# Performance work log

Hardware: AMD Instinct MI355X
Metric: run time of the kernel (lower is better)

Reference implementation:

```python
import jax, jax.numpy as jnp
import numpy as np

N, E, IN, H, G, OUT = 50000, 800000, 128, 128, 64, 10
HEADS, C = 4, 32  # per-head dim = H // HEADS so 4-head concat -> H (keeps chain dims consistent)


def setup_inputs() -> dict:
    key = jax.random.key(0)
    ks = jax.random.split(key, 16)
    p = lambda i, shape: jax.random.normal(ks[i], shape, jnp.float32) * 0.05
    return {
        "x": jax.random.normal(ks[0], (N, IN), jnp.float32),
        "edge_index": jax.random.randint(ks[1], (2, E), 0, N),
        "batch": jnp.sort(jax.random.randint(ks[2], (N,), 0, G)),
        "gcn_W": p(3, (IN, H)), "gcn_b": jnp.zeros((H,), jnp.float32),
        "gat_W": p(4, (H, HEADS * C)),
        "att_src": p(5, (HEADS, C)), "att_dst": p(6, (HEADS, C)),
        "gat_b": jnp.zeros((HEADS * C,), jnp.float32),
        "ec_W1": p(7, (2 * H, 128)), "ec_b1": jnp.zeros((128,), jnp.float32),
        "ec_W2": p(8, (128, H)), "ec_b2": jnp.zeros((H,), jnp.float32),
        "gin_W1": p(9, (H, 128)), "gin_b1": jnp.zeros((128,), jnp.float32),
        "gin_W2": p(10, (128, H)), "gin_b2": jnp.zeros((H,), jnp.float32),
        "gate_W1": p(11, (H, 128)), "gate_b1": jnp.zeros((128,), jnp.float32),
        "gate_W2": p(12, (128, 1)), "gate_b2": jnp.zeros((1,), jnp.float32),
        "fc_W": p(13, (H, OUT)), "fc_b": jnp.zeros((OUT,), jnp.float32),
    }


def reference(x, edge_index, batch, gcn_W, gcn_b, gat_W, att_src, att_dst, gat_b,
              ec_W1, ec_b1, ec_W2, ec_b2, gin_W1, gin_b1, gin_W2, gin_b2,
              gate_W1, gate_b1, gate_W2, gate_b2, fc_W, fc_b):
    src, dst = edge_index[0], edge_index[1]
    loop = jnp.arange(N)
    src_l = jnp.concatenate([src, loop])  # self loops for GCN / GAT
    dst_l = jnp.concatenate([dst, loop])

    deg = jax.ops.segment_sum(jnp.ones_like(dst_l, jnp.float32), dst_l, N)
    dinv = jnp.where(deg > 0, jax.lax.rsqrt(deg), 0.0)
    h = x @ gcn_W
    norm = dinv[src_l] * dinv[dst_l]  # [E+N]
    h = jax.ops.segment_sum(h[src_l] * norm[:, None], dst_l, N) + gcn_b
    h = jax.nn.relu(h)

    # ---- GATConv: 4 heads, per-target edge softmax, concat ----
    g = (h @ gat_W).reshape(N, HEADS, C)
    a_src = (g * att_src).sum(-1)  # [N, HEADS]
    a_dst = (g * att_dst).sum(-1)
    e = jax.nn.leaky_relu(a_src[src_l] + a_dst[dst_l], 0.2)  # [E+N, HEADS]
    e_max = jax.ops.segment_max(e, dst_l, N)
    e = jnp.exp(e - e_max[dst_l])
    e_sum = jax.ops.segment_sum(e, dst_l, N)
    alpha = e / (e_sum[dst_l] + 1e-16)
    h = jax.ops.segment_sum(g[src_l] * alpha[..., None], dst_l, N).reshape(N, HEADS * C) + gat_b
    h = jax.nn.elu(h)

    # ---- EdgeConv: nn([x_i, x_j - x_i]) with max aggregation ----
    msg = jnp.concatenate([h[dst], h[src] - h[dst]], axis=-1)  # [E, 2H]
    msg = jax.nn.relu(msg @ ec_W1 + ec_b1) @ ec_W2 + ec_b2
    agg = jax.ops.segment_max(msg, dst, N)
    h = jax.nn.relu(jnp.where(jnp.isfinite(agg), agg, 0.0))  # isolated nodes -> 0 (PyG scatter-max fill)

    # ---- GINConv (eps=0): nn(x + sum_j x_j) ----
    s = h + jax.ops.segment_sum(h[src], dst, N)
    h = jax.nn.relu(jax.nn.relu(s @ gin_W1 + gin_b1) @ gin_W2 + gin_b2)

    # ---- GlobalAttention pooling: per-graph softmax gating ----
    gate = jax.nn.relu(h @ gate_W1 + gate_b1) @ gate_W2 + gate_b2  # [N, 1]
    gmax = jax.ops.segment_max(gate, batch, G)
    ge = jnp.exp(gate - gmax[batch])
    gsum = jax.ops.segment_sum(ge, batch, G)
    w = ge / (gsum[batch] + 1e-16)
    pooled = jax.ops.segment_sum(w * h, batch, G)  # [G, H]

    out = pooled @ fc_W + fc_b
    return jax.nn.log_softmax(out, axis=1)
```

## Files before the change

### kernel.cpp

```cpp
#include <hip/hip_runtime.h>

#define H 128
#define OUTD 10

typedef short bf16x8 __attribute__((ext_vector_type(8)));
typedef float f32x4 __attribute__((ext_vector_type(4)));

__device__ __forceinline__ unsigned short f2bf(float x) {
  unsigned u = __float_as_uint(x);
  u += 0x7fffu + ((u >> 16) & 1u);
  return (unsigned short)(u >> 16);
}
__device__ __forceinline__ unsigned pack2bf(float a, float b) {
  return (unsigned)f2bf(a) | ((unsigned)f2bf(b) << 16);
}
__device__ __forceinline__ float bf2f(unsigned short u) {
  return __uint_as_float(((unsigned)u) << 16);
}
__device__ __forceinline__ float bflo(unsigned u) { return __uint_as_float(u << 16); }
__device__ __forceinline__ float bfhi(unsigned u) { return __uint_as_float(u & 0xffff0000u); }

__device__ __forceinline__ unsigned fenc(float x) {
  unsigned u = __float_as_uint(x);
  return (u & 0x80000000u) ? ~u : (u | 0x80000000u);
}
__device__ __forceinline__ float fdec(unsigned u) {
  u = (u & 0x80000000u) ? (u & 0x7fffffffu) : ~u;
  return __uint_as_float(u);
}

__global__ void prep_w(const float* __restrict__ gcnW, const float* __restrict__ gatW,
                       const float* __restrict__ ecW1, const float* __restrict__ ecW2,
                       const float* __restrict__ ginW1, const float* __restrict__ ginW2,
                       const float* __restrict__ gtW1, unsigned short* __restrict__ WT) {
  int f = blockIdx.x * 256 + threadIdx.x;
  if (f >= 8 * 16384) return;
  int m = f >> 14, idx = f & 16383;
  int j = idx >> 7, k = idx & 127;
  int src = k * 128 + j;
  float v;
  switch (m) {
    case 0: v = gcnW[src]; break;
    case 1: v = gatW[src]; break;
    case 2: v = ecW1[src] - ecW1[16384 + src]; break;
    case 3: v = ecW1[16384 + src]; break;
    case 4: v = ecW2[src]; break;
    case 5: v = ginW1[src]; break;
    case 6: v = ginW2[src]; break;
    default: v = gtW1[src]; break;
  }
  WT[f] = f2bf(v);
}

template <int IN_BF, int RELU, int BIAS>
__global__ __launch_bounds__(256) void dense_mfma(const void* __restrict__ Xv,
                                                  const unsigned short* __restrict__ WT,
                                                  const float* __restrict__ bias,
                                                  unsigned short* __restrict__ Y, int n) {
  __shared__ unsigned short tile[64][136];
  const int tid = threadIdx.x, lane = tid & 63, wave = tid >> 6;
  const int jl = lane & 15, kg = lane >> 4;
  const int base = blockIdx.x * 64;
  if (base >= n) return;
  const int nr = min(64, n - base);
  if (IN_BF) {
    const uint4* X4 = (const uint4*)Xv;
#pragma unroll
    for (int it = 0; it < 4; ++it) {
      int f = it * 256 + tid, r = f >> 4, q = f & 15;
      if (r < nr) *(uint4*)&tile[r][q * 8] = X4[(size_t)(base + r) * 16 + q];
    }
  } else {
    const float* X = (const float*)Xv;
#pragma unroll
    for (int it = 0; it < 16; ++it) {
      int f = it * 256 + tid, r = f >> 6, kp = f & 63;
      if (r < nr) {
        float2 v = *(const float2*)&X[(size_t)(base + r) * H + 2 * kp];
        *(unsigned*)&tile[r][2 * kp] = pack2bf(v.x, v.y);
      }
    }
  }
  __syncthreads();
  bf16x8 afrag[4];
#pragma unroll
  for (int kk = 0; kk < 4; ++kk)
    afrag[kk] = *(const bf16x8*)&tile[wave * 16 + jl][kk * 32 + kg * 8];
  f32x4 acc[8];
#pragma unroll
  for (int jt = 0; jt < 8; ++jt) {
    f32x4 c = {0.f, 0.f, 0.f, 0.f};
#pragma unroll
    for (int kk = 0; kk < 4; ++kk) {
      bf16x8 bf = *(const bf16x8*)&WT[(size_t)(jt * 16 + jl) * H + kk * 32 + kg * 8];
      c = __builtin_amdgcn_mfma_f32_16x16x32_bf16(afrag[kk], bf, c, 0, 0, 0);
    }
    if (BIAS) {
      float bb = bias[jt * 16 + jl];
#pragma unroll
      for (int r = 0; r < 4; ++r) c[r] += bb;
    }
    if (RELU) {
#pragma unroll
      for (int r = 0; r < 4; ++r) c[r] = fmaxf(c[r], 0.f);
    }
    acc[jt] = c;
  }
  __syncthreads();
#pragma unroll
  for (int jt = 0; jt < 8; ++jt)
#pragma unroll
    for (int r = 0; r < 4; ++r) tile[wave * 16 + kg * 4 + r][jt * 16 + jl] = f2bf(acc[jt][r]);
  __syncthreads();
#pragma unroll
  for (int it = 0; it < 4; ++it) {
    int f = it * 256 + tid, r = f >> 4, q = f & 15;
    if (r < nr) *(uint4*)&Y[(size_t)(base + r) * H + q * 8] = *(const uint4*)&tile[r][q * 8];
  }
}

__global__ __launch_bounds__(256) void dense_dual(const unsigned short* __restrict__ X,
                                                  const unsigned short* __restrict__ WT1,
                                                  const unsigned short* __restrict__ WT2,
                                                  const float* __restrict__ bias2,
                                                  unsigned short* __restrict__ Y1,
                                                  unsigned short* __restrict__ Y2, int n) {
  __shared__ unsigned short tile[64][136];
  const int tid = threadIdx.x, lane = tid & 63, wave = tid >> 6;
  const int jl = lane & 15, kg = lane >> 4;
  const int base = blockIdx.x * 64;
  if (base >= n) return;
  const int nr = min(64, n - base);
  const uint4* X4 = (const uint4*)X;
#pragma unroll
  for (int it = 0; it < 4; ++it) {
    int f = it * 256 + tid, r = f >> 4, q = f & 15;
    if (r < nr) *(uint4*)&tile[r][q * 8] = X4[(size_t)(base + r) * 16 + q];
  }
  __syncthreads();
  bf16x8 afrag[4];
#pragma unroll
  for (int kk = 0; kk < 4; ++kk)
    afrag[kk] = *(const bf16x8*)&tile[wave * 16 + jl][kk * 32 + kg * 8];
  f32x4 acc[8];
#pragma unroll
  for (int jt = 0; jt < 8; ++jt) {
    f32x4 c = {0.f, 0.f, 0.f, 0.f};
#pragma unroll
    for (int kk = 0; kk < 4; ++kk) {
      bf16x8 bf = *(const bf16x8*)&WT1[(size_t)(jt * 16 + jl) * H + kk * 32 + kg * 8];
      c = __builtin_amdgcn_mfma_f32_16x16x32_bf16(afrag[kk], bf, c, 0, 0, 0);
    }
    acc[jt] = c;
  }
  __syncthreads();
#pragma unroll
  for (int jt = 0; jt < 8; ++jt)
#pragma unroll
    for (int r = 0; r < 4; ++r) tile[wave * 16 + kg * 4 + r][jt * 16 + jl] = f2bf(acc[jt][r]);
  __syncthreads();
#pragma unroll
  for (int it = 0; it < 4; ++it) {
    int f = it * 256 + tid, r = f >> 4, q = f & 15;
    if (r < nr) *(uint4*)&Y1[(size_t)(base + r) * H + q * 8] = *(const uint4*)&tile[r][q * 8];
  }
  __syncthreads();
#pragma unroll
  for (int jt = 0; jt < 8; ++jt) {
    f32x4 c = {0.f, 0.f, 0.f, 0.f};
#pragma unroll
    for (int kk = 0; kk < 4; ++kk) {
      bf16x8 bf = *(const bf16x8*)&WT2[(size_t)(jt * 16 + jl) * H + kk * 32 + kg * 8];
      c = __builtin_amdgcn_mfma_f32_16x16x32_bf16(afrag[kk], bf, c, 0, 0, 0);
// ... 165 lines not shown
  for (int off = 1; off < 1024; off <<= 1) {
    int v = (t >= off) ? ls[t - off] : 0;
    __syncthreads();
    ls[t] += v;
    __syncthreads();
  }
  int run = (t > 0) ? ls[t - 1] : 0;
  for (int i = a; i < b; ++i) {
    row_ptr[i] = run;
    run += cnt[i];
  }
  if (t == 1023) row_ptr[n] = ls[1023];
}
__global__ void copy_int(const int* __restrict__ a, int* __restrict__ b, int n) {
  int i = blockIdx.x * 256 + threadIdx.x;
  if (i < n) b[i] = a[i];
}
__global__ void csr_fill(const int* __restrict__ ei, int* __restrict__ cursor,
                         int* __restrict__ csr_src, int* __restrict__ csr_dst, int E) {
  int e = blockIdx.x * 256 + threadIdx.x;
  if (e >= E) return;
  int s = ei[e], d = ei[(size_t)E + e];
  int p = atomicAdd(&cursor[d], 1);
  csr_src[p] = s;
  csr_dst[p] = d;
}
__global__ void dinv_kernel(const int* __restrict__ row_ptr, float* __restrict__ dinv, int n) {
  int i = blockIdx.x * 256 + threadIdx.x;
  if (i < n) dinv[i] = rsqrtf((float)(1 + row_ptr[i + 1] - row_ptr[i]));
}
__global__ void fill_u32(unsigned* p, unsigned v, size_t n) {
  size_t i = (size_t)blockIdx.x * 256 + threadIdx.x;
  if (i < n) p[i] = v;
}

__global__ __launch_bounds__(256) void gcn_gather(const unsigned short* __restrict__ h,
                                                  const float* __restrict__ dinv,
                                                  const int* __restrict__ row_ptr,
                                                  const int* __restrict__ csr_src,
                                                  const float* __restrict__ bias,
                                                  unsigned short* __restrict__ out, int n) {
  int node = blockIdx.x * 4 + (threadIdx.x >> 6);
  int lane = threadIdx.x & 63;
  if (node >= n) return;
  const unsigned* hu = (const unsigned*)h;
  float di = dinv[node];
  unsigned v = hu[(size_t)node * 64 + lane];
  float t0 = bflo(v) * di, t1 = bfhi(v) * di;
  int a = row_ptr[node], b = row_ptr[node + 1];
  int e = a;
  for (; e + 8 <= b; e += 8) {
    int sx[8];
#pragma unroll
    for (int i = 0; i < 8; ++i) sx[i] = csr_src[e + i];
    unsigned w[8];
    float dd[8];
#pragma unroll
    for (int i = 0; i < 8; ++i) w[i] = hu[(size_t)sx[i] * 64 + lane];
#pragma unroll
    for (int i = 0; i < 8; ++i) dd[i] = dinv[sx[i]];
#pragma unroll
    for (int i = 0; i < 8; ++i) {
      t0 = fmaf(bflo(w[i]), dd[i], t0);
      t1 = fmaf(bfhi(w[i]), dd[i], t1);
    }
  }
  for (; e < b; ++e) {
    int s = csr_src[e];
    float ds = dinv[s];
    unsigned w = hu[(size_t)s * 64 + lane];
    t0 = fmaf(bflo(w), ds, t0);
    t1 = fmaf(bfhi(w), ds, t1);
  }
  float y0 = fmaxf(fmaf(t0, di, bias[lane * 2]), 0.f);
  float y1 = fmaxf(fmaf(t1, di, bias[lane * 2 + 1]), 0.f);
  ((unsigned*)out)[(size_t)node * 64 + lane] = pack2bf(y0, y1);
}

__global__ void att_pre(const unsigned short* __restrict__ g, const float* __restrict__ attS,
                        const float* __restrict__ attD, float* __restrict__ asrc,
                        float* __restrict__ adst, int n) {
  int t = blockIdx.x * 256 + threadIdx.x;
  if (t >= n * 4) return;
  int i = t >> 2, hd = t & 3;
  const unsigned* gr = (const unsigned*)(g + (size_t)i * H + hd * 32);
  float s1 = 0.f, s2 = 0.f;
#pragma unroll
  for (int p = 0; p < 16; ++p) {
    unsigned u = gr[p];
    float a = bflo(u), b = bfhi(u);
    s1 = fmaf(a, attS[hd * 32 + 2 * p], fmaf(b, attS[hd * 32 + 2 * p + 1], s1));
    s2 = fmaf(a, attD[hd * 32 + 2 * p], fmaf(b, attD[hd * 32 + 2 * p + 1], s2));
  }
  asrc[t] = s1;
  adst[t] = s2;
}

__device__ __forceinline__ float lrelu_exp(float v) {
  v = v > 0.f ? v : 0.2f * v;
  return __expf(v);
}

__global__ __launch_bounds__(256) void gat_gather(const unsigned short* __restrict__ g,
                                                  const float* __restrict__ asrc,
                                                  const float* __restrict__ adst,
                                                  const int* __restrict__ row_ptr,
                                                  const int* __restrict__ csr_src,
                                                  const float* __restrict__ bias,
                                                  unsigned short* __restrict__ out, int n) {
  int node = blockIdx.x * 4 + (threadIdx.x >> 6);
  int lane = threadIdx.x & 63;
  if (node >= n) return;
  const int hd = lane >> 4;
  const unsigned* gu = (const unsigned*)g;
  float adc = adst[node * 4 + hd];
  float w = lrelu_exp(asrc[node * 4 + hd] + adc);
  unsigned u = gu[(size_t)node * 64 + lane];
  float acc0 = w * bflo(u), acc1 = w * bfhi(u), wsum = w;
  int a = row_ptr[node], b = row_ptr[node + 1];
  int e = a;
  for (; e + 8 <= b; e += 8) {
    int sx[8];
#pragma unroll
    for (int i = 0; i < 8; ++i) sx[i] = csr_src[e + i];
    unsigned uu[8];
#pragma unroll
    for (int i = 0; i < 8; ++i) uu[i] = gu[(size_t)sx[i] * 64 + lane];
    float ww[8];
#pragma unroll
    for (int i = 0; i < 8; ++i) ww[i] = lrelu_exp(asrc[sx[i] * 4 + hd] + adc);
#pragma unroll
    for (int i = 0; i < 8; ++i) {
      acc0 = fmaf(ww[i], bflo(uu[i]), acc0);
      acc1 = fmaf(ww[i], bfhi(uu[i]), acc1);
      wsum += ww[i];
    }
  }
  for (; e < b; ++e) {
    int s = csr_src[e];
    unsigned us = gu[(size_t)s * 64 + lane];
    float we = lrelu_exp(asrc[s * 4 + hd] + adc);
    acc0 = fmaf(we, bflo(us), acc0);
    acc1 = fmaf(we, bfhi(us), acc1);
    wsum += we;
  }
  float inv = 1.f / (wsum + 1e-16f);
  float r0 = acc0 * inv + bias[2 * lane];
  float r1 = acc1 * inv + bias[2 * lane + 1];
  r0 = r0 > 0.f ? r0 : expm1f(r0);
  r1 = r1 > 0.f ? r1 : expm1f(r1);
  ((unsigned*)out)[(size_t)node * 64 + lane] = pack2bf(r0, r1);
}

__global__ __launch_bounds__(256) void edgeconv_tile(const unsigned short* __restrict__ A,
                                                     const unsigned short* __restrict__ Bm,
                                                     const int* __restrict__ csr_src,
                                                     const int* __restrict__ csr_dst,
                                                     const unsigned short* __restrict__ W2T,
                                                     const float* __restrict__ b2,
                                                     unsigned* __restrict__ hec, int E) {
  __shared__ unsigned short buf[2][64][140];
  __shared__ int dbuf[2][64];
  const int tid = threadIdx.x, lane = tid & 63, wave = tid >> 6;
  const int jl = lane & 15, kg = lane >> 4;
  const int srow = tid >> 2, sq = tid & 3;
  float b2v[8];
#pragma unroll
  for (int jt = 0; jt < 8; ++jt) b2v[jt] = b2[jt * 16 + jl];

  const int tiles = (E + 63) >> 6;
  int t = blockIdx.x;
  if (t >= tiles) return;
  int cur = 0;
  {
    int base = t << 6;
    int ne = min(64, E - base);
    uint2 pk[8];
    if (srow < ne) {
      int d = csr_dst[base + srow], s = csr_src[base + srow];
      const uint2* Ar = (const uint2*)(A + (size_t)d * H + sq * 32);
      const uint2* Br = (const uint2*)(Bm + (size_t)s * H + sq * 32);
#pragma unroll
      for (int i = 0; i < 8; ++i) {
        uint2 va = Ar[i], vb = Br[i];
        pk[i].x = pack2bf(fmaxf(bflo(va.x) + bflo(vb.x), 0.f), fmaxf(bfhi(va.x) + bfhi(vb.x), 0.f));
        pk[i].y = pack2bf(fmaxf(bflo(va.y) + bflo(vb.y), 0.f), fmaxf(bfhi(va.y) + bfhi(vb.y), 0.f));
      }
    } else {
#pragma unroll
      for (int i = 0; i < 8; ++i) pk[i] = {0u, 0u};
    }
#pragma unroll
    for (int i = 0; i < 8; ++i) *(uint2*)&buf[0][srow][sq * 32 + i * 4] = pk[i];
    if (sq == 0) dbuf[0][srow] = (srow < ne) ? csr_dst[base + srow] : -1;
  }
  __syncthreads();

  for (; t < tiles; t += gridDim.x) {
    const int nt = t + gridDim.x;
    const bool havenext = nt < tiles;
    uint2 pk[8];
    if (havenext) {
      int base = nt << 6;
      int ne = min(64, E - base);
      if (srow < ne) {
        int d = csr_dst[base + srow], s = csr_src[base + srow];
        const uint2* Ar = (const uint2*)(A + (size_t)d * H + sq * 32);
        const uint2* Br = (const uint2*)(Bm + (size_t)s * H + sq * 32);
#pragma unroll
        for (int i = 0; i < 8; ++i) {
          uint2 va = Ar[i], vb = Br[i];
          pk[i].x =
              pack2bf(fmaxf(bflo(va.x) + bflo(vb.x), 0.f), fmaxf(bfhi(va.x) + bfhi(vb.x), 0.f));
          pk[i].y =
              pack2bf(fmaxf(bflo(va.y) + bflo(vb.y), 0.f), fmaxf(bfhi(va.y) + bfhi(vb.y), 0.f));
        }
      } else {
#pragma unroll
        for (int i = 0; i < 8; ++i) pk[i] = {0u, 0u};
      }
    }
    bf16x8 af[4];
#pragma unroll
    for (int kk = 0; kk < 4; ++kk)
      af[kk] = *(const bf16x8*)&buf[cur][wave * 16 + jl][kk * 32 + kg * 8];
    const int r0 = wave * 16 + kg * 4;
    const int d0 = dbuf[cur][r0 + 0], d1 = dbuf[cur][r0 + 1];
    const int d2 = dbuf[cur][r0 + 2], d3 = dbuf[cur][r0 + 3];
    f32x4 acc[8];
#pragma unroll
    for (int jt = 0; jt < 8; ++jt) {
      f32x4 c = {0.f, 0.f, 0.f, 0.f};
#pragma unroll
      for (int kk = 0; kk < 4; ++kk) {
        bf16x8 wf = *(const bf16x8*)&W2T[(size_t)(jt * 16 + jl) * H + kk * 32 + kg * 8];
        c = __builtin_amdgcn_mfma_f32_16x16x32_bf16(af[kk], wf, c, 0, 0, 0);
      }
      acc[jt] = c;
    }
    if (havenext) {
      int base = nt << 6;
      int ne = min(64, E - base);
#pragma unroll
      for (int i = 0; i < 8; ++i) *(uint2*)&buf[cur ^ 1][srow][sq * 32 + i * 4] = pk[i];
      if (sq == 0) dbuf[cur ^ 1][srow] = (srow < ne) ? csr_dst[base + srow] : -1;
    }
    __syncthreads();
#pragma unroll
    for (int jt = 0; jt < 8; ++jt) {
      const int col = jt * 16 + jl;
      f32x4 c = acc[jt];
      int cd = d0;
      float m = c[0];
      if (d1 != cd) {
        if (cd >= 0) atomicMax(&hec[(size_t)cd * H + col], fenc(m + b2v[jt]));
        cd = d1;
        m = c[1];
      } else
        m = fmaxf(m, c[1]);
      if (d2 != cd) {
        if (cd >= 0) atomicMax(&hec[(size_t)cd * H + col], fenc(m + b2v[jt]));
        cd = d2;
        m = c[2];
      } else
        m = fmaxf(m, c[2]);
      if (d3 != cd) {
        if (cd >= 0) atomicMax(&hec[(size_t)cd * H + col], fenc(m + b2v[jt]));
        cd = d3;
        m = c[3];
      } else
        m = fmaxf(m, c[3]);
      if (cd >= 0) atomicMax(&hec[(size_t)cd * H + col], fenc(m + b2v[jt]));
    }
    cur ^= 1;
  }
}

__global__ void ec_decode(const unsigned* __restrict__ hec, unsigned short* __restrict__ out,
                          size_t half) {
  size_t i = (size_t)blockIdx.x * 256 + threadIdx.x;
  if (i < half) {
    uint2 v = *(const uint2*)&hec[i * 2];
    ((unsigned*)out)[i] = pack2bf(fdec(v.x), fdec(v.y));
  }
}

__global__ __launch_bounds__(256) void gin_gather(const unsigned short* __restrict__ h,
                                                  const int* __restrict__ row_ptr,
                                                  const int* __restrict__ csr_src,
                                                  unsigned short* __restrict__ out, int n) {
  int node = blockIdx.x * 4 + (threadIdx.x >> 6);
  int lane = threadIdx.x & 63;
  if (node >= n) return;
  const unsigned* hu = (const unsigned*)h;
  unsigned v = hu[(size_t)node * 64 + lane];
  float t0 = bflo(v), t1 = bfhi(v);
  int a = row_ptr[node], b = row_ptr[node + 1];
  int e = a;
  for (; e + 8 <= b; e += 8) {
    int sx[8];
#pragma unroll
    for (int i = 0; i < 8; ++i) sx[i] = csr_src[e + i];
    unsigned w[8];
#pragma unroll
    for (int i = 0; i < 8; ++i) w[i] = hu[(size_t)sx[i] * 64 + lane];
#pragma unroll
    for (int i = 0; i < 8; ++i) {
      t0 += bflo(w[i]);
      t1 += bfhi(w[i]);
    }
  }
  for (; e < b; ++e) {
    int s = csr_src[e];
    unsigned w = hu[(size_t)s * 64 + lane];
    t0 += bflo(w);
    t1 += bfhi(w);
  }
  ((unsigned*)out)[(size_t)node * 64 + lane] = pack2bf(t0, t1);
}

__global__ void starts_kernel(const int* __restrict__ batch, int* __restrict__ starts, int n,
                              int G) {
  int i = blockIdx.x * 256 + threadIdx.x;
  if (i >= n) return;
  int b = batch[i];
  int bp = (i == 0) ? -1 : batch[i - 1];
  for (int g = bp + 1; g <= b; ++g) starts[g] = i;
  if (i == n - 1)
    for (int g = b + 1; g <= G; ++g) starts[g] = n;
}
__global__ __launch_bounds__(256) void pool_fused(float* __restrict__ gate,
                                                  const unsigned short* __restrict__ h4,
                                                  const int* __restrict__ starts,
                                                  const float* __restrict__ fcW,
                                                  const float* __restrict__ fcB,
                                                  float* __restrict__ out) {
  __shared__ float red[256];
  __shared__ float pl[128];
  int g = blockIdx.x, t = threadIdx.x;
  int s0 = starts[g], s1 = starts[g + 1];
  float m = -1e30f;
  for (int i = s0 + t; i < s1; i += 256) m = fmaxf(m, gate[i]);
  red[t] = m;
  __syncthreads();
  for (int off = 128; off; off >>= 1) {
    if (t < off) red[t] = fmaxf(red[t], red[t + off]);
    __syncthreads();
  }
  m = red[0];
  __syncthreads();
  float sm = 0.f;
  for (int i = s0 + t; i < s1; i += 256) {
    float ge = __expf(gate[i] - m);
    gate[i] = ge;
    sm += ge;
  }
  red[t] = sm;
  __syncthreads();
  for (int off = 128; off; off >>= 1) {
    if (t < off) red[t] += red[t + off];
    __syncthreads();
  }
  float inv = 1.f / (red[0] + 1e-16f);
  __syncthreads();
  int c = t & 127, half = t >> 7;
  float acc = 0.f;
  for (int i = s0 + half; i < s1; i += 2) acc = fmaf(gate[i], bf2f(h4[(size_t)i * H + c]), acc);
  red[t] = acc;
  __syncthreads();
  if (t < 128) pl[t] = (red[t] + red[t + 128]) * inv;
  __syncthreads();
  if (t < OUTD) {
    float o = fcB[t];
    for (int k = 0; k < 128; ++k) o = fmaf(pl[k], fcW[k * OUTD + t], o);
    red[t] = o;
  }
  __syncthreads();
  if (t == 0) {
    float mm = -1e30f;
    for (int j = 0; j < OUTD; ++j) mm = fmaxf(mm, red[j]);
    float s = 0.f;
    for (int j = 0; j < OUTD; ++j) s += __expf(red[j] - mm);
    float l = logf(s);
    for (int j = 0; j < OUTD; ++j) out[g * OUTD + j] = red[j] - mm - l;
  }
}

extern "C" void kernel_launch(void* const* d_in, const int* in_sizes, int n_in, void* d_out,
                              int out_size, void* d_ws, size_t ws_size, hipStream_t stream) {
  const float* x = (const float*)d_in[0];
  const int* ei = (const int*)d_in[1];
  const int* batch = (const int*)d_in[2];
  const float* gcnW = (const float*)d_in[3];
  const float* gcnB = (const float*)d_in[4];
  const float* gatW = (const float*)d_in[5];
  const float* attS = (const float*)d_in[6];
  const float* attD = (const float*)d_in[7];
  const float* gatB = (const float*)d_in[8];
  const float* ecW1 = (const float*)d_in[9];
  const float* ecB1 = (const float*)d_in[10];
  const float* ecW2 = (const float*)d_in[11];
  const float* ecB2 = (const float*)d_in[12];
  const float* ginW1 = (const float*)d_in[13];
  const float* ginB1 = (const float*)d_in[14];
  const float* ginW2 = (const float*)d_in[15];
  const float* ginB2 = (const float*)d_in[16];
  const float* gtW1 = (const float*)d_in[17];
  const float* gtB1 = (const float*)d_in[18];
  const float* gtW2 = (const float*)d_in[19];
  const float* gtB2 = (const float*)d_in[20];
  const float* fcW = (const float*)d_in[21];
  const float* fcB = (const float*)d_in[22];

  const int N = in_sizes[0] / H;
  const int E = in_sizes[1] / 2;
  const int G = out_size / OUTD;
  const size_t NH = (size_t)N * H;

  auto align16 = [](char* p) { return (char*)(((uintptr_t)p + 15) & ~(uintptr_t)15); };
  char* p = (char*)d_ws;
  unsigned* hec = (unsigned*)p;      p += NH * 4;
  float* dinv = (float*)p;           p += (size_t)N * 4;
  float* asrc = (float*)p;           p += (size_t)4 * N * 4;
  float* adst = (float*)p;           p += (size_t)4 * N * 4;
  float* gate = (float*)p;           p += (size_t)N * 4;
  int* starts = (int*)p;             p += (size_t)(G + 1) * 4;
  int* cnt = (int*)p;                p += (size_t)N * 4;
  int* row_ptr = (int*)p;            p += (size_t)(N + 1) * 4;
  int* cursor = (int*)p;             p += (size_t)N * 4;
  int* csr_src = (int*)p;            p += (size_t)E * 4;
  int* csr_dst = (int*)p;            p += (size_t)E * 4;
  p = align16(p);
  unsigned short* WT = (unsigned short*)p;  p += (size_t)8 * 16384 * 2;
  p = align16(p);
  unsigned short* T0 = (unsigned short*)p;  p += NH * 2;
  p = align16(p);
  unsigned short* T1 = (unsigned short*)p;  p += NH * 2;
  p = align16(p);
  unsigned short* T2 = (unsigned short*)p;  p += NH * 2;

  const unsigned short* gcnT = WT;
  const unsigned short* gatT = WT + 16384;
  const unsigned short* WaT = WT + 2 * 16384;
  const unsigned short* WbT = WT + 3 * 16384;
  const unsigned short* W2T = WT + 4 * 16384;
  const unsigned short* gin1T = WT + 5 * 16384;
  const unsigned short* gin2T = WT + 6 * 16384;
  const unsigned short* gt1T = WT + 7 * 16384;

  const int gN = (N + 255) / 256;
  const int gNH = (int)((NH + 255) / 256);
  const int gE = (E + 255) / 256;
  const int gDense = (N + 63) / 64;
  const int gW4 = (N + 3) / 4;

  prep_w<<<(8 * 16384 + 255) / 256, 256, 0, stream>>>(gcnW, gatW, ecW1, ecW2, ginW1, ginW2,
                                                      gtW1, WT);
  zero_int<<<gN, 256, 0, stream>>>(cnt, N);
  csr_count<<<gE, 256, 0, stream>>>(ei, cnt, E);
  scan50k<<<1, 1024, 0, stream>>>(cnt, row_ptr, N);
  copy_int<<<gN, 256, 0, stream>>>(row_ptr, cursor, N);
  csr_fill<<<gE, 256, 0, stream>>>(ei, cursor, csr_src, csr_dst, E);
  dinv_kernel<<<gN, 256, 0, stream>>>(row_ptr, dinv, N);

  dense_mfma<0, 0, 0><<<gDense, 256, 0, stream>>>(x, gcnT, nullptr, T0, N);
  gcn_gather<<<gW4, 256, 0, stream>>>(T0, dinv, row_ptr, csr_src, gcnB, T1, N);

  dense_mfma<1, 0, 0><<<gDense, 256, 0, stream>>>(T1, gatT, nullptr, T2, N);
  att_pre<<<(N * 4 + 255) / 256, 256, 0, stream>>>(T2, attS, attD, asrc, adst, N);
  gat_gather<<<gW4, 256, 0, stream>>>(T2, asrc, adst, row_ptr, csr_src, gatB, T0, N);

  dense_dual<<<gDense, 256, 0, stream>>>(T0, WaT, WbT, ecB1, T1, T2, N);
  fill_u32<<<gNH, 256, 0, stream>>>(hec, 0x80000000u, NH);
  edgeconv_tile<<<2048, 256, 0, stream>>>(T1, T2, csr_src, csr_dst, W2T, ecB2, hec, E);
  ec_decode<<<(int)((NH / 2 + 255) / 256), 256, 0, stream>>>(hec, T0, NH / 2);

  gin_gather<<<gW4, 256, 0, stream>>>(T0, row_ptr, csr_src, T1, N);
  dense_chain<<<gDense, 256, 0, stream>>>(T1, gin1T, ginB1, gin2T, ginB2, T2, N);

  dense_gate<<<gDense, 256, 0, stream>>>(T2, gt1T, gtB1, gtW2, gtB2, gate, N);
  starts_kernel<<<gN, 256, 0, stream>>>(batch, starts, N, G);
  pool_fused<<<G, 256, 0, stream>>>(gate, T2, starts, fcW, fcB, (float*)d_out);
}
```

Before: 813.6 us.

## Aggregate EdgeConv max per destination in LDS slots before global atomics

Edges in each 64-edge tile are sorted by destination, so the kernel now runs a wave-level scan that assigns each distinct destination in the tile to one of up to 16 shared-memory slots. Partial maxima go through LDS atomicMax, and a single pass then flushes each slot to global memory. Destinations whose whole CSR range lies inside the tile get a plain store; the others still use a global atomicMax. This cuts global atomic traffic, at the cost of an extra barrier, the scan, and LDS atomics in every tile.

```diff
diff --git a/kernel.cpp b/kernel.cpp
--- a/kernel.cpp
+++ b/kernel.cpp
@@ -494,17 +494,26 @@
                                                      const unsigned short* __restrict__ Bm,
                                                      const int* __restrict__ csr_src,
                                                      const int* __restrict__ csr_dst,
+                                                     const int* __restrict__ row_ptr,
                                                      const unsigned short* __restrict__ W2T,
                                                      const float* __restrict__ b2,
                                                      unsigned* __restrict__ hec, int E) {
   __shared__ unsigned short buf[2][64][140];
   __shared__ int dbuf[2][64];
+  __shared__ unsigned slots[16][128];
+  __shared__ int slotmap[2][64];
+  __shared__ int slot_dst2[2][16];
+  __shared__ int slot_comp2[2][16];
+  __shared__ int nslots2[2];
   const int tid = threadIdx.x, lane = tid & 63, wave = tid >> 6;
   const int jl = lane & 15, kg = lane >> 4;
   const int srow = tid >> 2, sq = tid & 3;
   float b2v[8];
 #pragma unroll
   for (int jt = 0; jt < 8; ++jt) b2v[jt] = b2[jt * 16 + jl];
+  const float b2c = b2[tid & 127];
+
+  for (int i = tid; i < 16 * 128; i += 256) ((unsigned*)slots)[i] = 0;
 
   const int tiles = (E + 63) >> 6;
   int t = blockIdx.x;
@@ -535,14 +544,16 @@
   __syncthreads();
 
   for (; t < tiles; t += gridDim.x) {
+    const int base = t << 6;
+    const int ne = min(64, E - base);
     const int nt = t + gridDim.x;
     const bool havenext = nt < tiles;
     uint2 pk[8];
     if (havenext) {
-      int base = nt << 6;
-      int ne = min(64, E - base);
-      if (srow < ne) {
-        int d = csr_dst[base + srow], s = csr_src[base + srow];
+      int nbase = nt << 6;
+      int nne = min(64, E - nbase);
+      if (srow < nne) {
+        int d = csr_dst[nbase + srow], s = csr_src[nbase + srow];
         const uint2* Ar = (const uint2*)(A + (size_t)d * H + sq * 32);
         const uint2* Br = (const uint2*)(Bm + (size_t)s * H + sq * 32);
 #pragma unroll
@@ -562,9 +573,6 @@
 #pragma unroll
     for (int kk = 0; kk < 4; ++kk)
       af[kk] = *(const bf16x8*)&buf[cur][wave * 16 + jl][kk * 32 + kg * 8];
-    const int r0 = wave * 16 + kg * 4;
-    const int d0 = dbuf[cur][r0 + 0], d1 = dbuf[cur][r0 + 1];
-    const int d2 = dbuf[cur][r0 + 2], d3 = dbuf[cur][r0 + 3];
     f32x4 acc[8];
 #pragma unroll
     for (int jt = 0; jt < 8; ++jt) {
@@ -577,38 +585,89 @@
       acc[jt] = c;
     }
     if (havenext) {
-      int base = nt << 6;
-      int ne = min(64, E - base);
+      int nbase = nt << 6;
+      int nne = min(64, E - nbase);
 #pragma unroll
       for (int i = 0; i < 8; ++i) *(uint2*)&buf[cur ^ 1][srow][sq * 32 + i * 4] = pk[i];
-      if (sq == 0) dbuf[cur ^ 1][srow] = (srow < ne) ? csr_dst[base + srow] : -1;
+      if (sq == 0) dbuf[cur ^ 1][srow] = (srow < nne) ? csr_dst[nbase + srow] : -1;
+    }
+    if (wave == 0) {
+      int r = lane;
+      int d = dbuf[cur][r];
+      int dp = (r == 0) ? -1234567 : dbuf[cur][r - 1];
+      int start = (r < ne && d != dp) ? 1 : 0;
+      int ps = start;
+#pragma unroll
+      for (int off = 1; off < 64; off <<= 1) {
+        int v = __shfl_up(ps, off);
+        if (lane >= off) ps += v;
+      }
+      int slot = ps - 1;
+      slotmap[cur][r] = (r < ne) ? slot : 255;
+      if (start && slot < 16) {
+        slot_dst2[cur][slot] = d;
+        int e0 = row_ptr[d], e1 = row_ptr[d + 1];
+        slot_comp2[cur][slot] = (e0 >= base && e1 <= base + ne) ? 1 : 0;
+      }
+      if (r == 63) nslots2[cur] = ps;
     }
     __syncthreads();
-#pragma unroll
-    for (int jt = 0; jt < 8; ++jt) {
-      const int col = jt * 16 + jl;
-      f32x4 c = acc[jt];
-      int cd = d0;
-      float m = c[0];
-      if (d1 != cd) {
-        if (cd >= 0) atomicMax(&hec[(size_t)cd * H + col], fenc(m + b2v[jt]));
-        cd = d1;
-        m = c[1];
-      } else
-        m = fmaxf(m, c[1]);
-      if (d2 != cd) {
-        if (cd >= 0) atomicMax(&hec[(size_t)cd * H + col], fenc(m + b2v[jt]));
-        cd = d2;
-        m = c[2];
-      } else
-        m = fmaxf(m, c[2]);
-      if (d3 != cd) {
-        if (cd >= 0) atomicMax(&hec[(size_t)cd * H + col], fenc(m + b2v[jt]));
-        cd = d3;
-        m = c[3];
-      } else
-        m = fmaxf(m, c[3]);
-      if (cd >= 0) atomicMax(&hec[(size_t)cd * H + col], fenc(m + b2v[jt]));
+    {
+      const int r0 = wave * 16 + kg * 4;
+      int dd[4], ss[4];
+#pragma unroll
+      for (int r = 0; r < 4; ++r) {
+        dd[r] = dbuf[cur][r0 + r];
+        ss[r] = slotmap[cur][r0 + r];
+      }
+#pragma unroll
+      for (int jt = 0; jt < 8; ++jt) {
+        const int col = jt * 16 + jl;
+        f32x4 c = acc[jt];
+        int cd = dd[0], cs = ss[0];
+        float cm = c[0];
+#pragma unroll
+        for (int r = 1; r < 4; ++r) {
+          if (dd[r] == cd) {
+            cm = fmaxf(cm, c[r]);
+          } else {
+            if (cd >= 0) {
+              if (cs < 16)
+                atomicMax(&slots[cs][col], fenc(cm));
+              else
+                atomicMax(&hec[(size_t)cd * H + col], fenc(cm + b2v[jt]));
+            }
+            cd = dd[r];
+            cs = ss[r];
+            cm = c[r];
+          }
+        }
+        if (cd >= 0) {
+          if (cs < 16)
+            atomicMax(&slots[cs][col], fenc(cm));
+          else
+            atomicMax(&hec[(size_t)cd * H + col], fenc(cm + b2v[jt]));
+        }
+      }
+    }
+    __syncthreads();
+    {
+      int ns = min(nslots2[cur], 16);
+      int col = tid & 127, sb = tid >> 7;
+#pragma unroll
+      for (int k = 0; k < 8; ++k) {
+        int s = sb + k * 2;
+        if (s < ns) {
+          unsigned v = slots[s][col];
+          slots[s][col] = 0;
+          float f = fdec(v) + b2c;
+          size_t off = (size_t)slot_dst2[cur][s] * H + col;
+          if (slot_comp2[cur][s])
+            hec[off] = fenc(fmaxf(f, 0.f));
+          else
+            atomicMax(&hec[off], fenc(f));
+        }
+      }
     }
     cur ^= 1;
   }
@@ -810,7 +869,7 @@
 
   dense_dual<<<gDense, 256, 0, stream>>>(T0, WaT, WbT, ecB1, T1, T2, N);
   fill_u32<<<gNH, 256, 0, stream>>>(hec, 0x80000000u, NH);
-  edgeconv_tile<<<2048, 256, 0, stream>>>(T1, T2, csr_src, csr_dst, W2T, ecB2, hec, E);
+  edgeconv_tile<<<2048, 256, 0, stream>>>(T1, T2, csr_src, csr_dst, row_ptr, W2T, ecB2, hec, E);
   ec_decode<<<(int)((NH / 2 + 255) / 256), 256, 0, stream>>>(hec, T0, NH / 2);
 
   gin_gather<<<gW4, 256, 0, stream>>>(T0, row_ptr, csr_src, T1, N);
```

After: 844.3 us. 1.04x slower.

## Split EdgeConv into gather/add-relu message kernel and streaming MFMA max kernel

Applied to the files above, without the earlier changes.

When workspace allows, EdgeConv is split into two kernels. The first gathers the two per-node projections, adds them, applies relu and writes an E×128 bf16 message buffer. The second streams that buffer contiguously through the MFMA and atomic-max stage. The aim is to take the irregular random gathers out of the MFMA loop. The price is writing and re-reading about 200MB of intermediate data plus an extra launch. The fused kernel also now interleaves the atomics with the MFMAs instead of holding all accumulators first, and uses a smaller LDS pad.

```diff
diff --git a/kernel.cpp b/kernel.cpp
--- a/kernel.cpp
+++ b/kernel.cpp
@@ -19,6 +19,9 @@
 }
 __device__ __forceinline__ float bflo(unsigned u) { return __uint_as_float(u << 16); }
 __device__ __forceinline__ float bfhi(unsigned u) { return __uint_as_float(u & 0xffff0000u); }
+__device__ __forceinline__ unsigned addrelu2(unsigned a, unsigned b) {
+  return pack2bf(fmaxf(bflo(a) + bflo(b), 0.f), fmaxf(bfhi(a) + bfhi(b), 0.f));
+}
 
 __device__ __forceinline__ unsigned fenc(float x) {
   unsigned u = __float_as_uint(x);
@@ -490,14 +493,36 @@
   ((unsigned*)out)[(size_t)node * 64 + lane] = pack2bf(r0, r1);
 }
 
-__global__ __launch_bounds__(256) void edgeconv_tile(const unsigned short* __restrict__ A,
-                                                     const unsigned short* __restrict__ Bm,
-                                                     const int* __restrict__ csr_src,
-                                                     const int* __restrict__ csr_dst,
-                                                     const unsigned short* __restrict__ W2T,
-                                                     const float* __restrict__ b2,
-                                                     unsigned* __restrict__ hec, int E) {
-  __shared__ unsigned short buf[2][64][140];
+__global__ __launch_bounds__(256) void ec_msg(const unsigned short* __restrict__ A,
+                                              const unsigned short* __restrict__ Bm,
+                                              const int* __restrict__ csr_src,
+                                              const int* __restrict__ csr_dst,
+                                              unsigned short* __restrict__ msg, int E) {
+  const int tid = threadIdx.x;
+  const int qid = tid >> 4;
+  const int ql = tid & 15;
+  for (int e0 = blockIdx.x * 16; e0 < E; e0 += gridDim.x * 16) {
+    int e = e0 + qid;
+    if (e < E) {
+      int d = csr_dst[e], s = csr_src[e];
+      uint4 va = *(const uint4*)(A + (size_t)d * H + ql * 8);
+      uint4 vb = *(const uint4*)(Bm + (size_t)s * H + ql * 8);
+      uint4 o;
+      o.x = addrelu2(va.x, vb.x);
+      o.y = addrelu2(va.y, vb.y);
+      o.z = addrelu2(va.z, vb.z);
+      o.w = addrelu2(va.w, vb.w);
+      *(uint4*)(msg + (size_t)e * H + ql * 8) = o;
+    }
+  }
+}
+
+__global__ __launch_bounds__(256) void edgeconv_stream(const unsigned short* __restrict__ msg,
+                                                       const int* __restrict__ csr_dst,
+                                                       const unsigned short* __restrict__ W2T,
+                                                       const float* __restrict__ b2,
+                                                       unsigned* __restrict__ hec, int E) {
+  __shared__ unsigned short buf[2][64][136];
   __shared__ int dbuf[2][64];
   const int tid = threadIdx.x, lane = tid & 63, wave = tid >> 6;
   const int jl = lane & 15, kg = lane >> 4;
@@ -513,23 +538,17 @@
   {
     int base = t << 6;
     int ne = min(64, E - base);
-    uint2 pk[8];
+    uint4 pk[4];
     if (srow < ne) {
-      int d = csr_dst[base + srow], s = csr_src[base + srow];
-      const uint2* Ar = (const uint2*)(A + (size_t)d * H + sq * 32);
-      const uint2* Br = (const uint2*)(Bm + (size_t)s * H + sq * 32);
-#pragma unroll
-      for (int i = 0; i < 8; ++i) {
-        uint2 va = Ar[i], vb = Br[i];
-        pk[i].x = pack2bf(fmaxf(bflo(va.x) + bflo(vb.x), 0.f), fmaxf(bfhi(va.x) + bfhi(vb.x), 0.f));
-        pk[i].y = pack2bf(fmaxf(bflo(va.y) + bflo(vb.y), 0.f), fmaxf(bfhi(va.y) + bfhi(vb.y), 0.f));
-      }
+#pragma unroll
+      for (int i = 0; i < 4; ++i)
+        pk[i] = *(const uint4*)&msg[(size_t)(base + srow) * H + sq * 32 + i * 8];
     } else {
 #pragma unroll
-      for (int i = 0; i < 8; ++i) pk[i] = {0u, 0u};
-    }
-#pragma unroll
-    for (int i = 0; i < 8; ++i) *(uint2*)&buf[0][srow][sq * 32 + i * 4] = pk[i];
+      for (int i = 0; i < 4; ++i) pk[i] = {0u, 0u, 0u, 0u};
+    }
+#pragma unroll
+    for (int i = 0; i < 4; ++i) *(uint4*)&buf[0][srow][sq * 32 + i * 8] = pk[i];
     if (sq == 0) dbuf[0][srow] = (srow < ne) ? csr_dst[base + srow] : -1;
   }
   __syncthreads();
@@ -537,25 +556,18 @@
   for (; t < tiles; t += gridDim.x) {
     const int nt = t + gridDim.x;
     const bool havenext = nt < tiles;
-    uint2 pk[8];
+    uint4 pk[4];
+    int nne = 0;
     if (havenext) {
-      int base = nt << 6;
-      int ne = min(64, E - base);
-      if (srow < ne) {
-        int d = csr_dst[base + srow], s = csr_src[base + srow];
-        const uint2* Ar = (const uint2*)(A + (size_t)d * H + sq * 32);
-        const uint2* Br = (const uint2*)(Bm + (size_t)s * H + sq * 32);
-#pragma unroll
-        for (int i = 0; i < 8; ++i) {
-          uint2 va = Ar[i], vb = Br[i];
-          pk[i].x =
-              pack2bf(fmaxf(bflo(va.x) + bflo(vb.x), 0.f), fmaxf(bfhi(va.x) + bfhi(vb.x), 0.f));
-          pk[i].y =
-              pack2bf(fmaxf(bflo(va.y) + bflo(vb.y), 0.f), fmaxf(bfhi(va.y) + bfhi(vb.y), 0.f));
-        }
+      int nbase = nt << 6;
+      nne = min(64, E - nbase);
+      if (srow < nne) {
+#pragma unroll
+        for (int i = 0; i < 4; ++i)
+          pk[i] = *(const uint4*)&msg[(size_t)(nbase + srow) * H + sq * 32 + i * 8];
       } else {
 #pragma unroll
-        for (int i = 0; i < 8; ++i) pk[i] = {0u, 0u};
+        for (int i = 0; i < 4; ++i) pk[i] = {0u, 0u, 0u, 0u};
       }
     }
     bf16x8 af[4];
@@ -565,7 +577,6 @@
     const int r0 = wave * 16 + kg * 4;
     const int d0 = dbuf[cur][r0 + 0], d1 = dbuf[cur][r0 + 1];
     const int d2 = dbuf[cur][r0 + 2], d3 = dbuf[cur][r0 + 3];
-    f32x4 acc[8];
 #pragma unroll
     for (int jt = 0; jt < 8; ++jt) {
       f32x4 c = {0.f, 0.f, 0.f, 0.f};
@@ -574,20 +585,7 @@
         bf16x8 wf = *(const bf16x8*)&W2T[(size_t)(jt * 16 + jl) * H + kk * 32 + kg * 8];
         c = __builtin_amdgcn_mfma_f32_16x16x32_bf16(af[kk], wf, c, 0, 0, 0);
       }
-      acc[jt] = c;
-    }
-    if (havenext) {
-      int base = nt << 6;
-      int ne = min(64, E - base);
-#pragma unroll
-      for (int i = 0; i < 8; ++i) *(uint2*)&buf[cur ^ 1][srow][sq * 32 + i * 4] = pk[i];
-      if (sq == 0) dbuf[cur ^ 1][srow] = (srow < ne) ? csr_dst[base + srow] : -1;
-    }
-    __syncthreads();
-#pragma unroll
-    for (int jt = 0; jt < 8; ++jt) {
       const int col = jt * 16 + jl;
-      f32x4 c = acc[jt];
       int cd = d0;
       float m = c[0];
       if (d1 != cd) {
@@ -610,6 +608,129 @@
         m = fmaxf(m, c[3]);
       if (cd >= 0) atomicMax(&hec[(size_t)cd * H + col], fenc(m + b2v[jt]));
     }
+    if (havenext) {
+      int nbase = nt << 6;
+#pragma unroll
+      for (int i = 0; i < 4; ++i) *(uint4*)&buf[cur ^ 1][srow][sq * 32 + i * 8] = pk[i];
+      if (sq == 0) dbuf[cur ^ 1][srow] = (srow < nne) ? csr_dst[nbase + srow] : -1;
+    }
+    __syncthreads();
+    cur ^= 1;
+  }
+}
+
+__global__ __launch_bounds__(256) void edgeconv_tile(const unsigned short* __restrict__ A,
+                                                     const unsigned short* __restrict__ Bm,
+                                                     const int* __restrict__ csr_src,
+                                                     const int* __restrict__ csr_dst,
+                                                     const unsigned short* __restrict__ W2T,
+                                                     const float* __restrict__ b2,
+                                                     unsigned* __restrict__ hec, int E) {
+  __shared__ unsigned short buf[2][64][136];
+  __shared__ int dbuf[2][64];
+  const int tid = threadIdx.x, lane = tid & 63, wave = tid >> 6;
+  const int jl = lane & 15, kg = lane >> 4;
+  const int srow = tid >> 2, sq = tid & 3;
+  float b2v[8];
+#pragma unroll
+  for (int jt = 0; jt < 8; ++jt) b2v[jt] = b2[jt * 16 + jl];
+
+  const int tiles = (E + 63) >> 6;
+  int t = blockIdx.x;
+  if (t >= tiles) return;
+  int cur = 0;
+  {
+    int base = t << 6;
+    int ne = min(64, E - base);
+    uint2 pk[8];
+    if (srow < ne) {
+      int d = csr_dst[base + srow], s = csr_src[base + srow];
+      const uint2* Ar = (const uint2*)(A + (size_t)d * H + sq * 32);
+      const uint2* Br = (const uint2*)(Bm + (size_t)s * H + sq * 32);
+#pragma unroll
+      for (int i = 0; i < 8; ++i) {
+        uint2 va = Ar[i], vb = Br[i];
+        pk[i].x = addrelu2(va.x, vb.x);
+        pk[i].y = addrelu2(va.y, vb.y);
+      }
+    } else {
+#pragma unroll
+      for (int i = 0; i < 8; ++i) pk[i] = {0u, 0u};
+    }
+#pragma unroll
+    for (int i = 0; i < 8; ++i) *(uint2*)&buf[0][srow][sq * 32 + i * 4] = pk[i];
+    if (sq == 0) dbuf[0][srow] = (srow < ne) ? csr_dst[base + srow] : -1;
+  }
+  __syncthreads();
+
+  for (; t < tiles; t += gridDim.x) {
+    const int nt = t + gridDim.x;
+    const bool havenext = nt < tiles;
+    uint2 pk[8];
+    if (havenext) {
+      int base = nt << 6;
+      int ne = min(64, E - base);
+      if (srow < ne) {
+        int d = csr_dst[base + srow], s = csr_src[base + srow];
+        const uint2* Ar = (const uint2*)(A + (size_t)d * H + sq * 32);
+        const uint2* Br = (const uint2*)(Bm + (size_t)s * H + sq * 32);
+#pragma unroll
+        for (int i = 0; i < 8; ++i) {
+          uint2 va = Ar[i], vb = Br[i];
+          pk[i].x = addrelu2(va.x, vb.x);
+          pk[i].y = addrelu2(va.y, vb.y);
+        }
+      } else {
+#pragma unroll
+        for (int i = 0; i < 8; ++i) pk[i] = {0u, 0u};
+      }
+    }
+    bf16x8 af[4];
+#pragma unroll
+    for (int kk = 0; kk < 4; ++kk)
+      af[kk] = *(const bf16x8*)&buf[cur][wave * 16 + jl][kk * 32 + kg * 8];
+    const int r0 = wave * 16 + kg * 4;
+    const int d0 = dbuf[cur][r0 + 0], d1 = dbuf[cur][r0 + 1];
+    const int d2 = dbuf[cur][r0 + 2], d3 = dbuf[cur][r0 + 3];
+#pragma unroll
+    for (int jt = 0; jt < 8; ++jt) {
+      f32x4 c = {0.f, 0.f, 0.f, 0.f};
+#pragma unroll
+      for (int kk = 0; kk < 4; ++kk) {
+        bf16x8 wf = *(const bf16x8*)&W2T[(size_t)(jt * 16 + jl) * H + kk * 32 + kg * 8];
+        c = __builtin_amdgcn_mfma_f32_16x16x32_bf16(af[kk], wf, c, 0, 0, 0);
+      }
+      const int col = jt * 16 + jl;
+      int cd = d0;
+      float m = c[0];
+      if (d1 != cd) {
+        if (cd >= 0) atomicMax(&hec[(size_t)cd * H + col], fenc(m + b2v[jt]));
+        cd = d1;
+        m = c[1];
+      } else
+        m = fmaxf(m, c[1]);
+      if (d2 != cd) {
+        if (cd >= 0) atomicMax(&hec[(size_t)cd * H + col], fenc(m + b2v[jt]));
+        cd = d2;
+        m = c[2];
+      } else
+        m = fmaxf(m, c[2]);
+      if (d3 != cd) {
+        if (cd >= 0) atomicMax(&hec[(size_t)cd * H + col], fenc(m + b2v[jt]));
+        cd = d3;
+        m = c[3];
+      } else
+        m = fmaxf(m, c[3]);
+      if (cd >= 0) atomicMax(&hec[(size_t)cd * H + col], fenc(m + b2v[jt]));
+    }
+    if (havenext) {
+      int base = nt << 6;
+      int ne = min(64, E - base);
+#pragma unroll
+      for (int i = 0; i < 8; ++i) *(uint2*)&buf[cur ^ 1][srow][sq * 32 + i * 4] = pk[i];
+      if (sq == 0) dbuf[cur ^ 1][srow] = (srow < ne) ? csr_dst[base + srow] : -1;
+    }
+    __syncthreads();
     cur ^= 1;
   }
 }
@@ -776,6 +897,10 @@
   unsigned short* T1 = (unsigned short*)p;  p += NH * 2;
   p = align16(p);
   unsigned short* T2 = (unsigned short*)p;  p += NH * 2;
+  p = align16(p);
+  unsigned short* msgbuf = (unsigned short*)p;
+  size_t needed_split = (size_t)(p - (char*)d_ws) + (size_t)E * H * 2 + 64;
+  const bool use_split = ws_size >= needed_split;
 
   const unsigned short* gcnT = WT;
   const unsigned short* gatT = WT + 16384;
@@ -810,7 +935,12 @@
 
   dense_dual<<<gDense, 256, 0, stream>>>(T0, WaT, WbT, ecB1, T1, T2, N);
   fill_u32<<<gNH, 256, 0, stream>>>(hec, 0x80000000u, NH);
-  edgeconv_tile<<<2048, 256, 0, stream>>>(T1, T2, csr_src, csr_dst, W2T, ecB2, hec, E);
+  if (use_split) {
+    ec_msg<<<2048, 256, 0, stream>>>(T1, T2, csr_src, csr_dst, msgbuf, E);
+    edgeconv_stream<<<2048, 256, 0, stream>>>(msgbuf, csr_dst, W2T, ecB2, hec, E);
+  } else {
+    edgeconv_tile<<<2048, 256, 0, stream>>>(T1, T2, csr_src, csr_dst, W2T, ecB2, hec, E);
+  }
   ec_decode<<<(int)((NH / 2 + 255) / 256), 256, 0, stream>>>(hec, T0, NH / 2);
 
   gin_gather<<<gW4, 256, 0, stream>>>(T0, row_ptr, csr_src, T1, N);
```

Result: no change. 811.3 us (-0.3%).

## Replace block-level LDS double-buffered edgeconv with per-wave register-direct MFMA tiles

Applied to the files above, without the earlier changes.

The EdgeConv edge kernel no longer stages 64-edge tiles through shared memory with double buffering and block barriers. Each wave now handles its own 16-edge tile, loading the gathered A/B rows straight into registers in the MFMA operand layout, applying add+ReLU in place, and running the MFMAs and atomic max without any LDS or __syncthreads. This removes LDS traffic and barrier stalls but gives up the explicit prefetch overlap, so latency hiding now relies on wave-level parallelism across the grid.

```diff
diff --git a/kernel.cpp b/kernel.cpp
--- a/kernel.cpp
+++ b/kernel.cpp
@@ -19,6 +19,9 @@
 }
 __device__ __forceinline__ float bflo(unsigned u) { return __uint_as_float(u << 16); }
 __device__ __forceinline__ float bfhi(unsigned u) { return __uint_as_float(u & 0xffff0000u); }
+__device__ __forceinline__ unsigned addrelu2(unsigned a, unsigned b) {
+  return pack2bf(fmaxf(bflo(a) + bflo(b), 0.f), fmaxf(bfhi(a) + bfhi(b), 0.f));
+}
 
 __device__ __forceinline__ unsigned fenc(float x) {
   unsigned u = __float_as_uint(x);
@@ -490,82 +493,65 @@
   ((unsigned*)out)[(size_t)node * 64 + lane] = pack2bf(r0, r1);
 }
 
-__global__ __launch_bounds__(256) void edgeconv_tile(const unsigned short* __restrict__ A,
+__global__ __launch_bounds__(256) void edgeconv_wave(const unsigned short* __restrict__ A,
                                                      const unsigned short* __restrict__ Bm,
                                                      const int* __restrict__ csr_src,
                                                      const int* __restrict__ csr_dst,
                                                      const unsigned short* __restrict__ W2T,
                                                      const float* __restrict__ b2,
                                                      unsigned* __restrict__ hec, int E) {
-  __shared__ unsigned short buf[2][64][140];
-  __shared__ int dbuf[2][64];
-  const int tid = threadIdx.x, lane = tid & 63, wave = tid >> 6;
+  const int lane = threadIdx.x & 63;
   const int jl = lane & 15, kg = lane >> 4;
-  const int srow = tid >> 2, sq = tid & 3;
+  const int wid0 = blockIdx.x * 4 + (threadIdx.x >> 6);
+  const int nw = gridDim.x * 4;
   float b2v[8];
 #pragma unroll
   for (int jt = 0; jt < 8; ++jt) b2v[jt] = b2[jt * 16 + jl];
-
-  const int tiles = (E + 63) >> 6;
-  int t = blockIdx.x;
-  if (t >= tiles) return;
-  int cur = 0;
-  {
-    int base = t << 6;
-    int ne = min(64, E - base);
-    uint2 pk[8];
-    if (srow < ne) {
-      int d = csr_dst[base + srow], s = csr_src[base + srow];
-      const uint2* Ar = (const uint2*)(A + (size_t)d * H + sq * 32);
-      const uint2* Br = (const uint2*)(Bm + (size_t)s * H + sq * 32);
-#pragma unroll
-      for (int i = 0; i < 8; ++i) {
-        uint2 va = Ar[i], vb = Br[i];
-        pk[i].x = pack2bf(fmaxf(bflo(va.x) + bflo(vb.x), 0.f), fmaxf(bfhi(va.x) + bfhi(vb.x), 0.f));
-        pk[i].y = pack2bf(fmaxf(bflo(va.y) + bflo(vb.y), 0.f), fmaxf(bfhi(va.y) + bfhi(vb.y), 0.f));
+  const int ntile = (E + 15) >> 4;
+
+  for (int t = wid0; t < ntile; t += nw) {
+    const int base = t << 4;
+    const int myrow = base + jl;
+    uint4 va[4], vb[4];
+    if (myrow < E) {
+      int s = csr_src[myrow], d = csr_dst[myrow];
+      const unsigned short* Arow = A + (size_t)d * H + kg * 8;
+      const unsigned short* Brow = Bm + (size_t)s * H + kg * 8;
+#pragma unroll
+      for (int kk = 0; kk < 4; ++kk) {
+        va[kk] = *(const uint4*)(Arow + kk * 32);
+        vb[kk] = *(const uint4*)(Brow + kk * 32);
       }
     } else {
 #pragma unroll
-      for (int i = 0; i < 8; ++i) pk[i] = {0u, 0u};
-    }
-#pragma unroll
-    for (int i = 0; i < 8; ++i) *(uint2*)&buf[0][srow][sq * 32 + i * 4] = pk[i];
-    if (sq == 0) dbuf[0][srow] = (srow < ne) ? csr_dst[base + srow] : -1;
-  }
-  __syncthreads();
-
-  for (; t < tiles; t += gridDim.x) {
-    const int nt = t + gridDim.x;
-    const bool havenext = nt < tiles;
-    uint2 pk[8];
-    if (havenext) {
-      int base = nt << 6;
-      int ne = min(64, E - base);
-      if (srow < ne) {
-        int d = csr_dst[base + srow], s = csr_src[base + srow];
-        const uint2* Ar = (const uint2*)(A + (size_t)d * H + sq * 32);
-        const uint2* Br = (const uint2*)(Bm + (size_t)s * H + sq * 32);
-#pragma unroll
-        for (int i = 0; i < 8; ++i) {
-          uint2 va = Ar[i], vb = Br[i];
-          pk[i].x =
-              pack2bf(fmaxf(bflo(va.x) + bflo(vb.x), 0.f), fmaxf(bfhi(va.x) + bfhi(vb.x), 0.f));
-          pk[i].y =
-              pack2bf(fmaxf(bflo(va.y) + bflo(vb.y), 0.f), fmaxf(bfhi(va.y) + bfhi(vb.y), 0.f));
-        }
+      for (int kk = 0; kk < 4; ++kk) va[kk] = vb[kk] = {0u, 0u, 0u, 0u};
+    }
+    int d0, d1, d2, d3;
+    {
+      int rb = base + kg * 4;
+      if (rb + 3 < E) {
+        int4 q = *(const int4*)(csr_dst + rb);
+        d0 = q.x;
+        d1 = q.y;
+        d2 = q.z;
+        d3 = q.w;
       } else {
-#pragma unroll
-        for (int i = 0; i < 8; ++i) pk[i] = {0u, 0u};
+        d0 = (rb + 0 < E) ? csr_dst[rb + 0] : -1;
+        d1 = (rb + 1 < E) ? csr_dst[rb + 1] : -1;
+        d2 = (rb + 2 < E) ? csr_dst[rb + 2] : -1;
+        d3 = (rb + 3 < E) ? csr_dst[rb + 3] : -1;
       }
     }
     bf16x8 af[4];
 #pragma unroll
-    for (int kk = 0; kk < 4; ++kk)
-      af[kk] = *(const bf16x8*)&buf[cur][wave * 16 + jl][kk * 32 + kg * 8];
-    const int r0 = wave * 16 + kg * 4;
-    const int d0 = dbuf[cur][r0 + 0], d1 = dbuf[cur][r0 + 1];
-    const int d2 = dbuf[cur][r0 + 2], d3 = dbuf[cur][r0 + 3];
-    f32x4 acc[8];
+    for (int kk = 0; kk < 4; ++kk) {
+      uint4 o;
+      o.x = addrelu2(va[kk].x, vb[kk].x);
+      o.y = addrelu2(va[kk].y, vb[kk].y);
+      o.z = addrelu2(va[kk].z, vb[kk].z);
+      o.w = addrelu2(va[kk].w, vb[kk].w);
+      af[kk] = *(bf16x8*)&o;
+    }
 #pragma unroll
     for (int jt = 0; jt < 8; ++jt) {
       f32x4 c = {0.f, 0.f, 0.f, 0.f};
@@ -574,20 +560,7 @@
         bf16x8 wf = *(const bf16x8*)&W2T[(size_t)(jt * 16 + jl) * H + kk * 32 + kg * 8];
         c = __builtin_amdgcn_mfma_f32_16x16x32_bf16(af[kk], wf, c, 0, 0, 0);
       }
-      acc[jt] = c;
-    }
-    if (havenext) {
-      int base = nt << 6;
-      int ne = min(64, E - base);
-#pragma unroll
-      for (int i = 0; i < 8; ++i) *(uint2*)&buf[cur ^ 1][srow][sq * 32 + i * 4] = pk[i];
-      if (sq == 0) dbuf[cur ^ 1][srow] = (srow < ne) ? csr_dst[base + srow] : -1;
-    }
-    __syncthreads();
-#pragma unroll
-    for (int jt = 0; jt < 8; ++jt) {
       const int col = jt * 16 + jl;
-      f32x4 c = acc[jt];
       int cd = d0;
       float m = c[0];
       if (d1 != cd) {
@@ -610,7 +583,6 @@
         m = fmaxf(m, c[3]);
       if (cd >= 0) atomicMax(&hec[(size_t)cd * H + col], fenc(m + b2v[jt]));
     }
-    cur ^= 1;
   }
 }
 
@@ -810,7 +782,7 @@
 
   dense_dual<<<gDense, 256, 0, stream>>>(T0, WaT, WbT, ecB1, T1, T2, N);
   fill_u32<<<gNH, 256, 0, stream>>>(hec, 0x80000000u, NH);
-  edgeconv_tile<<<2048, 256, 0, stream>>>(T1, T2, csr_src, csr_dst, W2T, ecB2, hec, E);
+  edgeconv_wave<<<2048, 256, 0, stream>>>(T1, T2, csr_src, csr_dst, W2T, ecB2, hec, E);
   ec_decode<<<(int)((NH / 2 + 255) / 256), 256, 0, stream>>>(hec, T0, NH / 2);
 
   gin_gather<<<gW4, 256, 0, stream>>>(T0, row_ptr, csr_src, T1, N);
```

After: 809.0 us. About the same (-0.6%).
